# Optimization experiments

Measured on AMD Instinct MI355X. Metric: run time of the kernel, lower is better.

## Reference

```python
import jax, jax.numpy as jnp
import numpy as np

DIM = 2048
NUM_EXPERTS = 4
EPS = 1e-6
SCALE = 3.0


def setup_inputs() -> dict:
    key = jax.random.key(0)
    k_x, k_w = jax.random.split(key)
    x = jax.random.normal(k_x, (4, 8192, DIM), dtype=jnp.float32)
    norm_weight = jnp.ones((DIM,), dtype=jnp.float32)
    router_weight = jax.random.normal(k_w, (NUM_EXPERTS, DIM), dtype=jnp.float32) * (1.0 / np.sqrt(DIM))
    return {"x": x, "norm_weight": norm_weight, "router_weight": router_weight}


def reference(x, norm_weight, router_weight):
    # RMSNorm over last dim
    rms = jnp.sqrt(jnp.mean(x * x, axis=-1, keepdims=True) + EPS)
    xn = x / rms * norm_weight
    # tiny router projection: [b, s, d] @ [e, d]^T -> [b, s, e]
    logits = jnp.einsum('bsd,ed->bse', xn, router_weight) * SCALE
    return jnp.tanh(logits)
```

## Files before the change

### kernel.cpp

```cpp
#include <hip/hip_runtime.h>
#include <cmath>

constexpr int   DIM   = 2048;
constexpr int   NEXP  = 4;
constexpr float EPS   = 1e-6f;
constexpr float SCALE = 3.0f;

typedef float f32x4 __attribute__((ext_vector_type(4)));

__global__ __launch_bounds__(256, 2)
void altup_router_kernel(const float* __restrict__ x,
                         const float* __restrict__ nw,
                         const float* __restrict__ rw,
                         float* __restrict__ out,
                         int nrows)
{
    const int tid    = threadIdx.x;
    const int lane   = tid & 63;
    const int wid    = tid >> 6;
    const int nwaves = gridDim.x * (blockDim.x >> 6);
    const int wave   = blockIdx.x * (blockDim.x >> 6) + wid;
    const int base   = lane * 4;

    f32x4 w[NEXP][8];
#pragma unroll
    for (int e = 0; e < NEXP; ++e) {
#pragma unroll
        for (int k = 0; k < 8; ++k) {
            const int d = k * 256 + base;
            const f32x4 r = *reinterpret_cast<const f32x4*>(rw + e * DIM + d);
            const f32x4 n = *reinterpret_cast<const f32x4*>(nw + d);
            w[e][k] = r * n;
        }
    }

    const int npairs = (nrows + 1) >> 1;

    for (int pr = wave; pr < npairs; pr += nwaves) {
        const int row  = pr * 2;
        const bool two = (row + 1) < nrows;

        const float* xr0 = x + (size_t)row * DIM;
        const float* xr1 = xr0 + (two ? DIM : 0);

        f32x4 av[8], bv[8];
#pragma unroll
        for (int k = 0; k < 8; ++k) {
            const int d = k * 256 + base;
            av[k] = __builtin_nontemporal_load(
                        reinterpret_cast<const f32x4*>(xr0 + d));
            bv[k] = __builtin_nontemporal_load(
                        reinterpret_cast<const f32x4*>(xr1 + d));
        }

        float acc[10] = {0.f};
#pragma unroll
        for (int k = 0; k < 8; ++k) {
            const f32x4 a = av[k];
            const f32x4 b = bv[k];

#pragma unroll
            for (int j = 0; j < 4; ++j) {
                acc[0] = fmaf(a[j], a[j], acc[0]);
                acc[5] = fmaf(b[j], b[j], acc[5]);
            }

#pragma unroll
            for (int e = 0; e < NEXP; ++e) {
                const f32x4 we = w[e][k];
#pragma unroll
                for (int j = 0; j < 4; ++j) {
                    acc[1 + e] = fmaf(a[j], we[j], acc[1 + e]);
                    acc[6 + e] = fmaf(b[j], we[j], acc[6 + e]);
                }
            }
        }

#pragma unroll
        for (int m = 32; m >= 1; m >>= 1) {
#pragma unroll
            for (int i = 0; i < 10; ++i)
                acc[i] += __shfl_xor(acc[i], m, 64);
        }

        if (lane == 0) {
            const float ir0 = rsqrtf(acc[0] * (1.0f / DIM) + EPS);
            f32x4 o0;
            o0.x = tanhf(acc[1] * ir0 * SCALE);
            o0.y = tanhf(acc[2] * ir0 * SCALE);
            o0.z = tanhf(acc[3] * ir0 * SCALE);
            o0.w = tanhf(acc[4] * ir0 * SCALE);
            reinterpret_cast<f32x4*>(out)[row] = o0;

            if (two) {
                const float ir1 = rsqrtf(acc[5] * (1.0f / DIM) + EPS);
                f32x4 o1;
                o1.x = tanhf(acc[6] * ir1 * SCALE);
                o1.y = tanhf(acc[7] * ir1 * SCALE);
                o1.z = tanhf(acc[8] * ir1 * SCALE);
                o1.w = tanhf(acc[9] * ir1 * SCALE);
                reinterpret_cast<f32x4*>(out)[row + 1] = o1;
            }
        }
    }
}

extern "C" void kernel_launch(void* const* d_in, const int* in_sizes, int n_in,
                              void* d_out, int out_size, void* d_ws, size_t ws_size,
                              hipStream_t stream)
{
    const float* x   = (const float*)d_in[0];
    const float* nw  = (const float*)d_in[1];
    const float* rw  = (const float*)d_in[2];
    float*       out = (float*)d_out;

    const int nrows  = in_sizes[0] / DIM;
    const int npairs = (nrows + 1) >> 1;

    int blocks = 512;
    const int max_blocks = (npairs + 3) / 4;
    if (blocks > max_blocks) blocks = max_blocks;
    if (blocks < 1) blocks = 1;

    hipLaunchKernelGGL(altup_router_kernel, dim3(blocks), dim3(256), 0, stream,
                       x, nw, rw, out, nrows);
}
```

Before: 49.95 us.

## Precompute fused weights and process four rows per wave with streamed weights

Adds a small pre-kernel that multiplies the norm weight into the router weights and stores the result in the workspace. The main kernel now reloads those fused weights from cache for each k-chunk instead of holding all 32 weight vectors in registers, and each wave handles four rows at once instead of two. Occupancy bounds rise from 2 to 4 blocks per SM to increase the number of memory loads in flight on this bandwidth-bound read of 256MB. The cost is an extra kernel launch and repeated L1/L2 weight loads on every iteration.

```diff
diff --git a/kernel.cpp b/kernel.cpp
--- a/kernel.cpp
+++ b/kernel.cpp
@@ -8,10 +8,21 @@
 
 typedef float f32x4 __attribute__((ext_vector_type(4)));
 
-__global__ __launch_bounds__(256, 2)
+__global__ void fuse_weights_kernel(const float* __restrict__ nw,
+                                    const float* __restrict__ rw,
+                                    float* __restrict__ fw)
+{
+    const int i = blockIdx.x * blockDim.x + threadIdx.x;
+    if (i < NEXP * DIM / 4) {
+        const f32x4 r = reinterpret_cast<const f32x4*>(rw)[i];
+        const f32x4 n = reinterpret_cast<const f32x4*>(nw)[i & (DIM / 4 - 1)];
+        reinterpret_cast<f32x4*>(fw)[i] = r * n;
+    }
+}
+
+__global__ __launch_bounds__(256, 4)
 void altup_router_kernel(const float* __restrict__ x,
-                         const float* __restrict__ nw,
-                         const float* __restrict__ rw,
+                         const float* __restrict__ fw,
                          float* __restrict__ out,
                          int nrows)
 {
@@ -22,56 +33,52 @@
     const int wave   = blockIdx.x * (blockDim.x >> 6) + wid;
     const int base   = lane * 4;
 
-    f32x4 w[NEXP][8];
+    const int nquads = (nrows + 3) >> 2;
+
+    for (int q = wave; q < nquads; q += nwaves) {
+        const int row0 = q * 4;
+
+        const float* xr[4];
 #pragma unroll
-    for (int e = 0; e < NEXP; ++e) {
+        for (int r = 0; r < 4; ++r) {
+            int rr = row0 + r;
+            if (rr > nrows - 1) rr = nrows - 1;
+            xr[r] = x + (size_t)rr * DIM;
+        }
+
+        float acc[4][5];
+#pragma unroll
+        for (int r = 0; r < 4; ++r)
+#pragma unroll
+            for (int i = 0; i < 5; ++i) acc[r][i] = 0.f;
+
 #pragma unroll
         for (int k = 0; k < 8; ++k) {
             const int d = k * 256 + base;
-            const f32x4 r = *reinterpret_cast<const f32x4*>(rw + e * DIM + d);
-            const f32x4 n = *reinterpret_cast<const f32x4*>(nw + d);
-            w[e][k] = r * n;
-        }
-    }
 
-    const int npairs = (nrows + 1) >> 1;
+            f32x4 wv[NEXP];
+#pragma unroll
+            for (int e = 0; e < NEXP; ++e)
+                wv[e] = *reinterpret_cast<const f32x4*>(fw + e * DIM + d);
 
-    for (int pr = wave; pr < npairs; pr += nwaves) {
-        const int row  = pr * 2;
-        const bool two = (row + 1) < nrows;
-
-        const float* xr0 = x + (size_t)row * DIM;
-        const float* xr1 = xr0 + (two ? DIM : 0);
-
-        f32x4 av[8], bv[8];
+            f32x4 xv[4];
 #pragma unroll
-        for (int k = 0; k < 8; ++k) {
-            const int d = k * 256 + base;
-            av[k] = __builtin_nontemporal_load(
-                        reinterpret_cast<const f32x4*>(xr0 + d));
-            bv[k] = __builtin_nontemporal_load(
-                        reinterpret_cast<const f32x4*>(xr1 + d));
-        }
-
-        float acc[10] = {0.f};
-#pragma unroll
-        for (int k = 0; k < 8; ++k) {
-            const f32x4 a = av[k];
-            const f32x4 b = bv[k];
+            for (int r = 0; r < 4; ++r)
+                xv[r] = __builtin_nontemporal_load(
+                            reinterpret_cast<const f32x4*>(xr[r] + d));
 
 #pragma unroll
-            for (int j = 0; j < 4; ++j) {
-                acc[0] = fmaf(a[j], a[j], acc[0]);
-                acc[5] = fmaf(b[j], b[j], acc[5]);
-            }
-
+            for (int r = 0; r < 4; ++r) {
+                const f32x4 a = xv[r];
 #pragma unroll
-            for (int e = 0; e < NEXP; ++e) {
-                const f32x4 we = w[e][k];
+                for (int j = 0; j < 4; ++j)
+                    acc[r][0] = fmaf(a[j], a[j], acc[r][0]);
 #pragma unroll
-                for (int j = 0; j < 4; ++j) {
-                    acc[1 + e] = fmaf(a[j], we[j], acc[1 + e]);
-                    acc[6 + e] = fmaf(b[j], we[j], acc[6 + e]);
+                for (int e = 0; e < NEXP; ++e) {
+                    const f32x4 we = wv[e];
+#pragma unroll
+                    for (int j = 0; j < 4; ++j)
+                        acc[r][1 + e] = fmaf(a[j], we[j], acc[r][1 + e]);
                 }
             }
         }
@@ -79,27 +86,25 @@
 #pragma unroll
         for (int m = 32; m >= 1; m >>= 1) {
 #pragma unroll
-            for (int i = 0; i < 10; ++i)
-                acc[i] += __shfl_xor(acc[i], m, 64);
+            for (int r = 0; r < 4; ++r)
+#pragma unroll
+                for (int i = 0; i < 5; ++i)
+                    acc[r][i] += __shfl_xor(acc[r][i], m, 64);
         }
 
         if (lane == 0) {
-            const float ir0 = rsqrtf(acc[0] * (1.0f / DIM) + EPS);
-            f32x4 o0;
-            o0.x = tanhf(acc[1] * ir0 * SCALE);
-            o0.y = tanhf(acc[2] * ir0 * SCALE);
-            o0.z = tanhf(acc[3] * ir0 * SCALE);
-            o0.w = tanhf(acc[4] * ir0 * SCALE);
-            reinterpret_cast<f32x4*>(out)[row] = o0;
-
-            if (two) {
-                const float ir1 = rsqrtf(acc[5] * (1.0f / DIM) + EPS);
-                f32x4 o1;
-                o1.x = tanhf(acc[6] * ir1 * SCALE);
-                o1.y = tanhf(acc[7] * ir1 * SCALE);
-                o1.z = tanhf(acc[8] * ir1 * SCALE);
-                o1.w = tanhf(acc[9] * ir1 * SCALE);
-                reinterpret_cast<f32x4*>(out)[row + 1] = o1;
+#pragma unroll
+            for (int r = 0; r < 4; ++r) {
+                const int rr = row0 + r;
+                if (rr < nrows) {
+                    const float ir = rsqrtf(acc[r][0] * (1.0f / DIM) + EPS);
+                    f32x4 o;
+                    o.x = tanhf(acc[r][1] * ir * SCALE);
+                    o.y = tanhf(acc[r][2] * ir * SCALE);
+                    o.z = tanhf(acc[r][3] * ir * SCALE);
+                    o.w = tanhf(acc[r][4] * ir * SCALE);
+                    *reinterpret_cast<f32x4*>(out + (size_t)rr * 4) = o;
+                }
             }
         }
     }
@@ -113,15 +118,20 @@
     const float* nw  = (const float*)d_in[1];
     const float* rw  = (const float*)d_in[2];
     float*       out = (float*)d_out;
+    float*       fw  = (float*)d_ws;
 
-    const int nrows  = in_sizes[0] / DIM;
-    const int npairs = (nrows + 1) >> 1;
+    const int nrows = in_sizes[0] / DIM;
+
+    hipLaunchKernelGGL(fuse_weights_kernel, dim3(8), dim3(256), 0, stream,
+                       nw, rw, fw);
+
+    const int nquads = (nrows + 3) >> 2;
 
     int blocks = 512;
-    const int max_blocks = (npairs + 3) / 4;
+    const int max_blocks = (nquads + 3) / 4;
     if (blocks > max_blocks) blocks = max_blocks;
     if (blocks < 1) blocks = 1;
 
     hipLaunchKernelGGL(altup_router_kernel, dim3(blocks), dim3(256), 0, stream,
-                       x, nw, rw, out, nrows);
+                       x, fw, out, nrows);
 }
```

After: 136.3 us. 2.73x slower.
